# Kernel optimization log

Hardware: AMD Instinct MI355X
Metric: run time of the kernel (lower is better)

Reference implementation:

```python
import jax, jax.numpy as jnp
import numpy as np

EPS = 1e-6
CHUNK = 128  # chunk size for the causal linear-attention scan


def elu_plus_one(x):
    return jax.nn.elu(x) + 1.0


def causal_linear_attention(q, k, v):
    # out_t = (sq_t @ cumsum_{j<=t} sk_j v_j^T) / (sq_t . cumsum_{j<=t} sk_j), clamped
    B, S, D = q.shape
    sq = elu_plus_one(q)
    sk = elu_plus_one(k)
    N = S // CHUNK
    # [N, B, C, D] chunked layout for scan over chunks
    sq_c = sq.reshape(B, N, CHUNK, D).transpose(1, 0, 2, 3)
    sk_c = sk.reshape(B, N, CHUNK, D).transpose(1, 0, 2, 3)
    v_c = v.reshape(B, N, CHUNK, D).transpose(1, 0, 2, 3)
    mask = jnp.tril(jnp.ones((CHUNK, CHUNK), dtype=q.dtype))  # inclusive causal

    def step(carry, inp):
        S_kv, z = carry  # [B,D,D], [B,D] running sums from previous chunks
        sqi, ski, vi = inp
        A = jnp.einsum('bid,bjd->bij', sqi, ski) * mask  # intra-chunk causal scores
        num = jnp.einsum('bij,bje->bie', A, vi) + jnp.einsum('bid,bde->bie', sqi, S_kv)
        den = A.sum(-1) + jnp.einsum('bid,bd->bi', sqi, z)
        out = num / jnp.clip(den, EPS, None)[..., None]
        S_kv = S_kv + jnp.einsum('bcd,bce->bde', ski, vi)
        z = z + ski.sum(axis=1)
        return (S_kv, z), out

    init = (jnp.zeros((B, D, D), q.dtype), jnp.zeros((B, D), q.dtype))
    _, outs = jax.lax.scan(step, init, (sq_c, sk_c, v_c))
    return outs.transpose(1, 0, 2, 3).reshape(B, S, D)


def setup_inputs() -> dict:
    key = jax.random.key(0)
    ks = jax.random.split(key, 8)
    B, S, D = 2, 2048, 1024
    scale = 1.0 / np.sqrt(D)  # realistic init scale for the D x D projections
    return {
        'hidden_states': jax.random.normal(ks[0], (B, S, D), jnp.float32),
        'w_q': jax.random.normal(ks[1], (D, D), jnp.float32) * scale,
        'w_k': jax.random.normal(ks[2], (D, D), jnp.float32) * scale,
        'w_v': jax.random.normal(ks[3], (D, D), jnp.float32) * scale,
        'w_o': jax.random.normal(ks[4], (D, D), jnp.float32) * scale,
        'gate': jnp.zeros((1,), jnp.float32),
        'memory': jax.random.uniform(ks[5], (D, D), jnp.float32) * 0.01,
        'memory_norm': jax.random.uniform(ks[6], (D,), jnp.float32),
    }


def reference(hidden_states, w_q, w_k, w_v, w_o, gate, memory, memory_norm):
    # Projections (torch Linear: x @ W^T)
    q = hidden_states @ w_q.T
    k = hidden_states @ w_k.T
    v = hidden_states @ w_v.T

    # Retrieve from compressive memory (single bank)
    sigma_q = elu_plus_one(q)
    a_mem = sigma_q @ memory
    norm = jnp.clip(sigma_q @ memory_norm, EPS, None)[..., None]
    active = (memory_norm.sum() >= EPS).astype(q.dtype)
    memory_output = active * (a_mem / norm)

    local_output = causal_linear_attention(q, k, v)

    g = jax.nn.sigmoid(gate)  # [1], broadcasts
    output = g * memory_output + (1.0 - g) * local_output
    return output @ w_o.T
```

## Files before the change

### kernel.cpp

```cpp
#include <hip/hip_runtime.h>
#include <cstddef>

#define EPSF 1e-6f

constexpr int D   = 1024;
constexpr int Bv  = 2;
constexpr int S   = 2048;
constexpr int M   = Bv * S;
constexpr int CH  = 256;
constexpr int NCH = S / CH;

constexpr int TSZ  = 128 * 32;
constexpr int TA64 = 64 * 32;

typedef __attribute__((ext_vector_type(8))) short short8;
typedef __attribute__((ext_vector_type(4))) float floatx4;

__device__ __forceinline__ float elu1(float x) { return x > 0.f ? x + 1.f : __expf(x); }
__device__ __forceinline__ float sigmoidf_(float x) { return 1.f / (1.f + __expf(-x)); }
__device__ __forceinline__ unsigned short f2bf(float x) {
    unsigned u = __float_as_uint(x);
    return (unsigned short)((u + 0x7fffu + ((u >> 16) & 1u)) >> 16);
}
__device__ __forceinline__ float bf2f(unsigned short h) {
    return __uint_as_float(((unsigned)h) << 16);
}
__device__ __forceinline__ float wave_reduce(float x) {
#pragma unroll
    for (int off = 32; off > 0; off >>= 1) x += __shfl_down(x, off);
    return x;
}

__device__ __forceinline__ void gl_lds16(const unsigned short* g, unsigned short* l) {
    __builtin_amdgcn_global_load_lds(
        (const __attribute__((address_space(1))) void*)g,
        (__attribute__((address_space(3))) void*)l, 16, 0, 0);
}

__device__ __forceinline__ void stage128x32(const unsigned short* g, int stride,
                                            unsigned short* lds, int wave, int lane) {
    const int t   = (wave << 6) + lane;
    const int row = t >> 2;
    const int cb  = (t & 3) << 3;
    unsigned short* l0 = lds + (wave << 9);
    gl_lds16(g + (size_t)row * stride + cb, l0);
    gl_lds16(g + (size_t)(row + 64) * stride + cb, l0 + 2048);
}

__device__ __forceinline__ void stage64x32(const unsigned short* g, int stride,
                                           unsigned short* lds, int wave, int lane) {
    const int t   = (wave << 6) + lane;
    const int row = t >> 2;
    const int cb  = (t & 3) << 3;
    gl_lds16(g + (size_t)row * stride + cb, lds + (wave << 9));
}

__device__ __forceinline__ void mfma_step(const unsigned short* As, const unsigned short* Bs,
                                          int wm, int wn, int fr, int fo, floatx4 acc[4][4]) {
    short8 af[4], bf[4];
#pragma unroll
    for (int i = 0; i < 4; ++i) af[i] = *(const short8*)&As[(wm + i * 16 + fr) * 32 + fo];
#pragma unroll
    for (int j = 0; j < 4; ++j) bf[j] = *(const short8*)&Bs[(wn + j * 16 + fr) * 32 + fo];
#pragma unroll
    for (int i = 0; i < 4; ++i)
#pragma unroll
        for (int j = 0; j < 4; ++j)
            acc[i][j] = __builtin_amdgcn_mfma_f32_16x16x32_bf16(af[i], bf[j], acc[i][j], 0, 0, 0);
}

__device__ __forceinline__ void mfma_step64d(const unsigned short* As, const unsigned short* Bs,
                                             int wm, int wn, int fr, int fo,
                                             floatx4 acc[2][4], floatx4 accd[2], short8 bones) {
    short8 af[2], bf[4];
#pragma unroll
    for (int i = 0; i < 2; ++i) af[i] = *(const short8*)&As[(wm + i * 16 + fr) * 32 + fo];
#pragma unroll
    for (int j = 0; j < 4; ++j) bf[j] = *(const short8*)&Bs[(wn + j * 16 + fr) * 32 + fo];
#pragma unroll
    for (int i = 0; i < 2; ++i) {
#pragma unroll
        for (int j = 0; j < 4; ++j)
            acc[i][j] = __builtin_amdgcn_mfma_f32_16x16x32_bf16(af[i], bf[j], acc[i][j], 0, 0, 0);
        accd[i] = __builtin_amdgcn_mfma_f32_16x16x32_bf16(af[i], bones, accd[i], 0, 0, 0);
    }
}

__device__ __forceinline__ void mfma_step64(const unsigned short* As, const unsigned short* Bs,
                                            int wm, int wn, int fr, int fo, floatx4 acc[2][4]) {
    short8 af[2], bf[4];
#pragma unroll
    for (int i = 0; i < 2; ++i) af[i] = *(const short8*)&As[(wm + i * 16 + fr) * 32 + fo];
#pragma unroll
    for (int j = 0; j < 4; ++j) bf[j] = *(const short8*)&Bs[(wn + j * 16 + fr) * 32 + fo];
#pragma unroll
    for (int i = 0; i < 2; ++i)
#pragma unroll
        for (int j = 0; j < 4; ++j)
            acc[i][j] = __builtin_amdgcn_mfma_f32_16x16x32_bf16(af[i], bf[j], acc[i][j], 0, 0, 0);
}

__device__ __forceinline__ void gemm_loop_db(const unsigned short* Ag, int strideA,
                                             const unsigned short* Bg, int strideB, int Kk,
                                             unsigned short* As, unsigned short* Bs,
                                             int wave, int lane, int wm, int wn, int fr, int fo,
                                             floatx4 acc[4][4]) {
    __syncthreads();
    stage128x32(Ag, strideA, As, wave, lane);
    stage128x32(Bg, strideB, Bs, wave, lane);
    int buf = 0;
    for (int k0 = 32; k0 < Kk; k0 += 32) {
        __syncthreads();
        const int nb = buf ^ 1;
        stage128x32(Ag + k0, strideA, As + nb * TSZ, wave, lane);
        stage128x32(Bg + k0, strideB, Bs + nb * TSZ, wave, lane);
        mfma_step(As + buf * TSZ, Bs + buf * TSZ, wm, wn, fr, fo, acc);
        buf = nb;
    }
    __syncthreads();
    mfma_step(As + buf * TSZ, Bs + buf * TSZ, wm, wn, fr, fo, acc);
}

__device__ __forceinline__ void gemm_loop_db64d(const unsigned short* Ag, int strideA,
                                                const unsigned short* Bg, int strideB, int Kk,
                                                unsigned short* As, unsigned short* Bs,
                                                int wave, int lane, int wm, int wn, int fr, int fo,
                                                floatx4 acc[2][4], floatx4 accd[2], short8 bones) {
    __syncthreads();
    stage64x32(Ag, strideA, As, wave, lane);
    stage128x32(Bg, strideB, Bs, wave, lane);
    int buf = 0;
    for (int k0 = 32; k0 < Kk; k0 += 32) {
        __syncthreads();
        const int nb = buf ^ 1;
        stage64x32(Ag + k0, strideA, As + nb * TA64, wave, lane);
        stage128x32(Bg + k0, strideB, Bs + nb * TSZ, wave, lane);
        mfma_step64d(As + buf * TA64, Bs + buf * TSZ, wm, wn, fr, fo, acc, accd, bones);
        buf = nb;
    }
    __syncthreads();
    mfma_step64d(As + buf * TA64, Bs + buf * TSZ, wm, wn, fr, fo, acc, accd, bones);
}

__device__ __forceinline__ void gemm_loop_db64(const unsigned short* Ag, int strideA,
                                               const unsigned short* Bg, int strideB, int Kk,
                                               unsigned short* As, unsigned short* Bs,
                                               int wave, int lane, int wm, int wn, int fr, int fo,
                                               floatx4 acc[2][4]) {
    __syncthreads();
    stage64x32(Ag, strideA, As, wave, lane);
    stage128x32(Bg, strideB, Bs, wave, lane);
    int buf = 0;
    for (int k0 = 32; k0 < Kk; k0 += 32) {
        __syncthreads();
        const int nb = buf ^ 1;
        stage64x32(Ag + k0, strideA, As + nb * TA64, wave, lane);
        stage128x32(Bg + k0, strideB, Bs + nb * TSZ, wave, lane);
        mfma_step64(As + buf * TA64, Bs + buf * TSZ, wm, wn, fr, fo, acc);
        buf = nb;
    }
    __syncthreads();
    mfma_step64(As + buf * TA64, Bs + buf * TSZ, wm, wn, fr, fo, acc);
}

__global__ __launch_bounds__(256) void prep(const float* __restrict__ h,
                                            const float* __restrict__ w_q, const float* __restrict__ w_k,
                                            const float* __restrict__ w_v, const float* __restrict__ w_o,
                                            const float* __restrict__ memory,
                                            unsigned short* __restrict__ h_b,
                                            unsigned short* __restrict__ wq_b, unsigned short* __restrict__ wk_b,
                                            unsigned short* __restrict__ wv_b, unsigned short* __restrict__ wo_b,
                                            unsigned short* __restrict__ memT)
{
    __shared__ unsigned short T[64][72];
    const int id = blockIdx.x, tid = threadIdx.x;
    if (id < 4096) {
        const size_t i = ((size_t)id * 256 + tid) * 4;
        float4 v = *(const float4*)(h + i);
        ushort4 o; o.x = f2bf(v.x); o.y = f2bf(v.y); o.z = f2bf(v.z); o.w = f2bf(v.w);
        *(ushort4*)(h_b + i) = o;
    } else if (id < 8192) {
        const int t = id - 4096, which = t >> 10;
        const float* in = (which == 0) ? w_q : (which == 1) ? w_k : (which == 2) ? w_v : w_o;
        unsigned short* out = (which == 0) ? wq_b : (which == 1) ? wk_b : (which == 2) ? wv_b : wo_b;
        const size_t i = ((size_t)(t & 1023) * 256 + tid) * 4;
        float4 v = *(const float4*)(in + i);
        ushort4 o; o.x = f2bf(v.x); o.y = f2bf(v.y); o.z = f2bf(v.z); o.w = f2bf(v.w);
        *(ushort4*)(out + i) = o;
    } else {
        const int t = id - 8192;
        const int d0 = (t >> 4) * 64, e0 = (t & 15) * 64;
        const int r = tid >> 4, c4 = (tid & 15) * 4;
        for (int rr = r; rr < 64; rr += 16) {
            float4 v = *(const float4*)(memory + (size_t)(d0 + rr) * D + e0 + c4);
            T[rr][c4 + 0] = f2bf(v.x); T[rr][c4 + 1] = f2bf(v.y);
            T[rr][c4 + 2] = f2bf(v.z); T[rr][c4 + 3] = f2bf(v.w);
        }
        __syncthreads();
        for (int rr = r; rr < 64; rr += 16) {
            ushort4 o;
            o.x = T[c4 + 0][rr]; o.y = T[c4 + 1][rr];
            o.z = T[c4 + 2][rr]; o.w = T[c4 + 3][rr];
            *(ushort4*)(memT + (size_t)(e0 + rr) * D + d0 + c4) = o;
        }
    }
}

__global__ __launch_bounds__(256) void proj_fused(const unsigned short* __restrict__ h_b,
                                                  const unsigned short* __restrict__ wq,
                                                  const unsigned short* __restrict__ wk,
                                                  const unsigned short* __restrict__ wv,
                                                  unsigned short* __restrict__ sq,
                                                  unsigned short* __restrict__ sk,
                                                  unsigned short* __restrict__ v)
{
    __shared__ unsigned short As[2 * TSZ], Bs[2 * TSZ];
    const int id = blockIdx.x;
    const int x = id & 7, y = id >> 3;
    const int strip = x + 8 * (y % 12);
    const int n     = y / 12;
    const int sub = strip >> 5, m = strip & 31;
    const int m0 = m * 128, n0 = n * 128;
    const unsigned short* B = (sub == 0) ? wq : (sub == 1) ? wk : wv;
    unsigned short* C = (sub == 0) ? sq : (sub == 1) ? sk : v;

    const int tid = threadIdx.x, wave = tid >> 6, lane = tid & 63;
    const int wm = (wave >> 1) * 64, wn = (wave & 1) * 64;
    const int fr = lane & 15, fo = (lane >> 4) * 8;
    const int q4 = (lane >> 4) * 4;

    floatx4 acc[4][4] = {};
    gemm_loop_db(h_b + (size_t)m0 * D, D, B + (size_t)n0 * D, D, D,
                 As, Bs, wave, lane, wm, wn, fr, fo, acc);

#pragma unroll
    for (int i = 0; i < 4; ++i)
#pragma unroll
        for (int j = 0; j < 4; ++j) {
            const int col = n0 + wn + j * 16 + fr;
#pragma unroll
            for (int r = 0; r < 4; ++r) {
                const int row = m0 + wm + i * 16 + q4 + r;
                float val = acc[i][j][r];
                if (sub < 2) val = elu1(val);
                C[(size_t)row * D + col] = f2bf(val);
            }
        }
}

__global__ __launch_bounds__(256) void stage2(const unsigned short* __restrict__ sq,
                                              const unsigned short* __restrict__ sk,
                                              const unsigned short* __restrict__ memT,
                                              const unsigned short* __restrict__ v_b,
                                              const float* __restrict__ mnorm,
                                              const float* __restrict__ gate,
                                              unsigned short* __restrict__ combm,
                                              unsigned short* __restrict__ Sbuf2,
                                              unsigned short* __restrict__ vT,
                                              float* __restrict__ rowscale)
{
    __shared__ unsigned short As[2 * TSZ], Bs[2 * TSZ];
    const int id = blockIdx.x, tid = threadIdx.x;
    const int wave = tid >> 6, lane = tid & 63;
    const int wm = (wave >> 1) * 64, wn = (wave & 1) * 64;
    const int fr = lane & 15, fo = (lane >> 4) * 8;
    const int q4 = (lane >> 4) * 4;

    if (id < 256) {
        const int x = id & 7, y = id >> 3;
        const int m0 = (x + 8 * (y & 3)) * 128;
        const int n0 = (y >> 2) * 128;
        floatx4 acc[4][4] = {};
        gemm_loop_db(sq + (size_t)m0 * D, D, memT + (size_t)n0 * D, D, D,
                     As, Bs, wave, lane, wm, wn, fr, fo, acc);
#pragma unroll
        for (int i = 0; i < 4; ++i)
#pragma unroll
            for (int j = 0; j < 4; ++j) {
                const int col = n0 + wn + j * 16 + fr;
#pragma unroll
                for (int r = 0; r < 4; ++r)
                    combm[(size_t)(m0 + wm + i * 16 + q4 + r) * D + col] = f2bf(acc[i][j][r]);
            }
    } else if (id < 544) {
        const int t = id - 256;
        const int b = t / 144, rem = t % 144;
        const int p = rem >> 2, tt = rem & 3;
        const int it = tt >> 1, jt = tt & 1;
        int c = 0;
        while ((c + 1) * (c + 2) / 2 <= p) ++c;
        const int j = p - c * (c + 1) / 2;
        unsigned short* Srow0 = Sbuf2 + (size_t)(b * NCH + c) * CH * S;

        if (j == c && jt > it) {
            const int row = it * 128 + (tid >> 1);
            unsigned short* zp = Srow0 + (size_t)row * S + j * CH + jt * 128 + (tid & 1) * 64;
            uint4 z4 = make_uint4(0, 0, 0, 0);
#pragma unroll
            for (int i = 0; i < 8; ++i) *(uint4*)(zp + i * 8) = z4;
            return;
        }
        floatx4 acc[4][4] = {};
        gemm_loop_db(sq + ((size_t)b * S + (size_t)c * CH + it * 128) * D, D,
                     sk + ((size_t)b * S + (size_t)j * CH + jt * 128) * D, D, D,
                     As, Bs, wave, lane, wm, wn, fr, fo, acc);
        const bool diag = (j == c && it == jt);
#pragma unroll
        for (int i = 0; i < 4; ++i)
#pragma unroll
            for (int jj = 0; jj < 4; ++jj) {
                const int col = jt * 128 + wn + jj * 16 + fr;
#pragma unroll
                for (int r = 0; r < 4; ++r) {
                    const int row = it * 128 + wm + i * 16 + q4 + r;
                    float val = acc[i][jj][r];
                    if (diag && col > row) val = 0.f;
                    Srow0[(size_t)row * S + j * CH + col] = f2bf(val);
                }
            }
    } else if (id < 1568) {
        unsigned short (*T)[72] = (unsigned short(*)[72])As;
        const int t = id - 544;
        const int b = t >> 9, rem = t & 511;
        const int s0 = (rem >> 4) * 64, d0 = (rem & 15) * 64;
        const int r = tid >> 4, c4 = (tid & 15) * 4;
        const unsigned short* ip = v_b + (size_t)b * S * D;
        for (int rr = r; rr < 64; rr += 16) {
            ushort4 vv = *(const ushort4*)(ip + (size_t)(s0 + rr) * D + d0 + c4);
            T[rr][c4 + 0] = vv.x; T[rr][c4 + 1] = vv.y; T[rr][c4 + 2] = vv.z; T[rr][c4 + 3] = vv.w;
        }
        __syncthreads();
        unsigned short* op = vT + (size_t)b * D * S;
        for (int rr = r; rr < 64; rr += 16) {
            ushort4 o;
            o.x = T[c4 + 0][rr]; o.y = T[c4 + 1][rr];
            o.z = T[c4 + 2][rr]; o.w = T[c4 + 3][rr];
            *(ushort4*)(op + (size_t)(d0 + rr) * S + s0 + c4) = o;
        }
    } else {
        const int row = (id - 1568) * 4 + wave;
        const unsigned short* sr = sq + (size_t)row * D;
        float dot = 0.f, msum = 0.f;
        for (int d = lane; d < D; d += 64) {
            float mn = mnorm[d];
            dot += bf2f(sr[d]) * mn;
            msum += mn;
        }
        dot = wave_reduce(dot);
        msum = wave_reduce(msum);
        if (lane == 0) {
            const float g = sigmoidf_(gate[0]);
            const float active = (msum >= EPSF) ? 1.f : 0.f;
            rowscale[row] = g * active / fmaxf(dot, EPSF);
        }
    }
}

__global__ __launch_bounds__(256) void pv64(const unsigned short* __restrict__ Sbuf2,
                                            const unsigned short* __restrict__ vT,
                                            const float* __restrict__ rowscale,
                                            const float* __restrict__ gate,
                                            unsigned short* __restrict__ combm)
{
    __shared__ unsigned short As2[2 * TA64], Bs2[2 * TSZ];
    const int id = blockIdx.x, tid = threadIdx.x;
    const int wave = tid >> 6, lane = tid & 63;
    const int wm = (wave >> 1) * 32, wn = (wave & 1) * 64;
    const int fr = lane & 15, fo = (lane >> 4) * 8;
    const int q4 = (lane >> 4) * 4;

    const int x = id & 7, y = id >> 3;
    const int g_ = x + 8 * (y & 7);
    const int e  = y >> 3;
    const int b = g_ >> 5;
    const int rem = g_ & 31;
    const int c = (NCH - 1) - (rem >> 2);
    const int i0 = (rem & 3) * 64, e0 = e * 128;

    const short one_bf = (short)0x3F80;
    short8 bones = {one_bf, one_bf, one_bf, one_bf, one_bf, one_bf, one_bf, one_bf};

    floatx4 acc[2][4] = {};
    floatx4 accd[2] = {};
    gemm_loop_db64d(Sbuf2 + ((size_t)(b * NCH + c) * CH + i0) * S, S,
                    vT + (size_t)b * D * S + (size_t)e0 * S, S, (c + 1) * CH,
                    As2, Bs2, wave, lane, wm, wn, fr, fo, acc, accd, bones);

    const float g = sigmoidf_(gate[0]);
    const float wloc = 1.f - g;
#pragma unroll
    for (int i = 0; i < 2; ++i)
#pragma unroll
        for (int j = 0; j < 4; ++j) {
            const int col = e0 + wn + j * 16 + fr;
#pragma unroll
            for (int r = 0; r < 4; ++r) {
                const int li = i0 + wm + i * 16 + q4 + r;
                const int rg = b * S + c * CH + li;
                const float inv = wloc / fmaxf(accd[i][r], EPSF);
                const size_t idx = (size_t)rg * D + col;
                combm[idx] = f2bf(bf2f(combm[idx]) * rowscale[rg] + acc[i][j][r] * inv);
            }
        }
}

__global__ __launch_bounds__(256) void outproj64(const unsigned short* __restrict__ A,
                                                 const unsigned short* __restrict__ wo,
                                                 float* __restrict__ out)
{
    __shared__ unsigned short As2[2 * TA64], Bs2[2 * TSZ];
    const int id = blockIdx.x, tid = threadIdx.x;
    const int wave = tid >> 6, lane = tid & 63;
    const int wm = (wave >> 1) * 32, wn = (wave & 1) * 64;
    const int fr = lane & 15, fo = (lane >> 4) * 8;
    const int q4 = (lane >> 4) * 4;

    const int x = id & 7, y = id >> 3;
    const int m0 = (x + 8 * (y & 7)) * 64;
    const int n0 = (y >> 3) * 128;

    floatx4 acc[2][4] = {};
    gemm_loop_db64(A + (size_t)m0 * D, D, wo + (size_t)n0 * D, D, D,
                   As2, Bs2, wave, lane, wm, wn, fr, fo, acc);

#pragma unroll
    for (int i = 0; i < 2; ++i)
#pragma unroll
        for (int j = 0; j < 4; ++j) {
            const int col = n0 + wn + j * 16 + fr;
#pragma unroll
            for (int r = 0; r < 4; ++r)
                out[(size_t)(m0 + wm + i * 16 + q4 + r) * D + col] = acc[i][j][r];
        }
}

extern "C" void kernel_launch(void* const* d_in, const int* in_sizes, int n_in,
                              void* d_out, int out_size, void* d_ws, size_t ws_size,
                              hipStream_t stream)
{
    const float* h      = (const float*)d_in[0];
    const float* w_q    = (const float*)d_in[1];
    const float* w_k    = (const float*)d_in[2];
    const float* w_v    = (const float*)d_in[3];
    const float* w_o    = (const float*)d_in[4];
    const float* gate   = (const float*)d_in[5];
    const float* memory = (const float*)d_in[6];
    const float* mnorm  = (const float*)d_in[7];
    float* out = (float*)d_out;

    unsigned short* h_b   = (unsigned short*)d_ws;
    unsigned short* wq_b  = h_b + (size_t)M * D;
    unsigned short* wk_b  = wq_b + (size_t)D * D;
    unsigned short* wv_b  = wk_b + (size_t)D * D;
    unsigned short* wo_b  = wv_b + (size_t)D * D;
    unsigned short* memT  = wo_b + (size_t)D * D;
    unsigned short* sq_b  = memT + (size_t)D * D;
    unsigned short* sk_b  = sq_b + (size_t)M * D;
    unsigned short* v_b   = sk_b + (size_t)M * D;
    unsigned short* vT    = v_b + (size_t)M * D;
    unsigned short* Sbuf2 = vT + (size_t)M * D;
    unsigned short* combm = Sbuf2 + (size_t)Bv * NCH * CH * S;
    float* rowscale = (float*)(combm + (size_t)M * D);

    dim3 blk(256);

    prep<<<8448, blk, 0, stream>>>(h, w_q, w_k, w_v, w_o, memory,
                                   h_b, wq_b, wk_b, wv_b, wo_b, memT);
    proj_fused<<<768, blk, 0, stream>>>(h_b, wq_b, wk_b, wv_b, sq_b, sk_b, v_b);
    stage2<<<2592, blk, 0, stream>>>(sq_b, sk_b, memT, v_b, mnorm, gate,
                                     combm, Sbuf2, vT, rowscale);
    pv64<<<512, blk, 0, stream>>>(Sbuf2, vT, rowscale, gate, combm);
    outproj64<<<512, blk, 0, stream>>>(combm, wo_b, out);
}
```

Baseline: 230.1 us.

## Double K-tile depth to 64 with XOR-swizzled LDS layout in all GEMMs

Every GEMM main loop now advances K by 64 per stage instead of 32, which halves the number of barriers and loop iterations. The staging writes each 16-byte chunk into a column position XOR-swizzled by row so that fragment reads with a 64-element row stride avoid LDS bank conflicts. The cost is double the LDS footprint per block, which may lower occupancy, plus a longer prologue and epilogue per tile.

```diff
diff --git a/kernel.cpp b/kernel.cpp
--- a/kernel.cpp
+++ b/kernel.cpp
@@ -10,8 +10,8 @@
 constexpr int CH  = 256;
 constexpr int NCH = S / CH;
 
-constexpr int TSZ  = 128 * 32;
-constexpr int TA64 = 64 * 32;
+constexpr int TSZ  = 128 * 64;
+constexpr int TA64 = 64 * 64;
 
 typedef __attribute__((ext_vector_type(8))) short short8;
 typedef __attribute__((ext_vector_type(4))) float floatx4;
@@ -37,130 +37,152 @@
         (__attribute__((address_space(3))) void*)l, 16, 0, 0);
 }
 
-__device__ __forceinline__ void stage128x32(const unsigned short* g, int stride,
+
+__device__ __forceinline__ void stage128x64(const unsigned short* g, int stride,
                                             unsigned short* lds, int wave, int lane) {
-    const int t   = (wave << 6) + lane;
-    const int row = t >> 2;
-    const int cb  = (t & 3) << 3;
-    unsigned short* l0 = lds + (wave << 9);
-    gl_lds16(g + (size_t)row * stride + cb, l0);
-    gl_lds16(g + (size_t)(row + 64) * stride + cb, l0 + 2048);
-}
-
-__device__ __forceinline__ void stage64x32(const unsigned short* g, int stride,
+    const int base = (wave << 6) + lane;
+    const int c8   = (lane & 7) ^ (lane >> 3);
+#pragma unroll
+    for (int q = 0; q < 4; ++q) {
+        const int P   = (q << 8) + base;
+        const int row = P >> 3;
+        gl_lds16(g + (size_t)row * stride + (c8 << 3), lds + (q << 11) + (wave << 9));
+    }
+}
+
+__device__ __forceinline__ void stage64x64(const unsigned short* g, int stride,
                                            unsigned short* lds, int wave, int lane) {
-    const int t   = (wave << 6) + lane;
-    const int row = t >> 2;
-    const int cb  = (t & 3) << 3;
-    gl_lds16(g + (size_t)row * stride + cb, lds + (wave << 9));
+    const int base = (wave << 6) + lane;
+    const int c8   = (lane & 7) ^ (lane >> 3);
+#pragma unroll
+    for (int q = 0; q < 2; ++q) {
+        const int P   = (q << 8) + base;
+        const int row = P >> 3;
+        gl_lds16(g + (size_t)row * stride + (c8 << 3), lds + (q << 11) + (wave << 9));
+    }
 }
 
 __device__ __forceinline__ void mfma_step(const unsigned short* As, const unsigned short* Bs,
-                                          int wm, int wn, int fr, int fo, floatx4 acc[4][4]) {
-    short8 af[4], bf[4];
-#pragma unroll
-    for (int i = 0; i < 4; ++i) af[i] = *(const short8*)&As[(wm + i * 16 + fr) * 32 + fo];
-#pragma unroll
-    for (int j = 0; j < 4; ++j) bf[j] = *(const short8*)&Bs[(wn + j * 16 + fr) * 32 + fo];
-#pragma unroll
-    for (int i = 0; i < 4; ++i)
-#pragma unroll
-        for (int j = 0; j < 4; ++j)
-            acc[i][j] = __builtin_amdgcn_mfma_f32_16x16x32_bf16(af[i], bf[j], acc[i][j], 0, 0, 0);
+                                          int wm, int wn, int fr, int g, floatx4 acc[4][4]) {
+    const int x7 = fr & 7;
+#pragma unroll
+    for (int s = 0; s < 2; ++s) {
+        const int off = ((g + 4 * s) ^ x7) << 3;
+        short8 af[4], bf[4];
+#pragma unroll
+        for (int i = 0; i < 4; ++i) af[i] = *(const short8*)&As[(wm + i * 16 + fr) * 64 + off];
+#pragma unroll
+        for (int j = 0; j < 4; ++j) bf[j] = *(const short8*)&Bs[(wn + j * 16 + fr) * 64 + off];
+#pragma unroll
+        for (int i = 0; i < 4; ++i)
+#pragma unroll
+            for (int j = 0; j < 4; ++j)
+                acc[i][j] = __builtin_amdgcn_mfma_f32_16x16x32_bf16(af[i], bf[j], acc[i][j], 0, 0, 0);
+    }
 }
 
 __device__ __forceinline__ void mfma_step64d(const unsigned short* As, const unsigned short* Bs,
-                                             int wm, int wn, int fr, int fo,
+                                             int wm, int wn, int fr, int g,
                                              floatx4 acc[2][4], floatx4 accd[2], short8 bones) {
-    short8 af[2], bf[4];
-#pragma unroll
-    for (int i = 0; i < 2; ++i) af[i] = *(const short8*)&As[(wm + i * 16 + fr) * 32 + fo];
-#pragma unroll
-    for (int j = 0; j < 4; ++j) bf[j] = *(const short8*)&Bs[(wn + j * 16 + fr) * 32 + fo];
-#pragma unroll
-    for (int i = 0; i < 2; ++i) {
-#pragma unroll
-        for (int j = 0; j < 4; ++j)
-            acc[i][j] = __builtin_amdgcn_mfma_f32_16x16x32_bf16(af[i], bf[j], acc[i][j], 0, 0, 0);
-        accd[i] = __builtin_amdgcn_mfma_f32_16x16x32_bf16(af[i], bones, accd[i], 0, 0, 0);
+    const int x7 = fr & 7;
+#pragma unroll
+    for (int s = 0; s < 2; ++s) {
+        const int off = ((g + 4 * s) ^ x7) << 3;
+        short8 af[2], bf[4];
+#pragma unroll
+        for (int i = 0; i < 2; ++i) af[i] = *(const short8*)&As[(wm + i * 16 + fr) * 64 + off];
+#pragma unroll
+        for (int j = 0; j < 4; ++j) bf[j] = *(const short8*)&Bs[(wn + j * 16 + fr) * 64 + off];
+#pragma unroll
+        for (int i = 0; i < 2; ++i) {
+#pragma unroll
+            for (int j = 0; j < 4; ++j)
+                acc[i][j] = __builtin_amdgcn_mfma_f32_16x16x32_bf16(af[i], bf[j], acc[i][j], 0, 0, 0);
+            accd[i] = __builtin_amdgcn_mfma_f32_16x16x32_bf16(af[i], bones, accd[i], 0, 0, 0);
+        }
     }
 }
 
 __device__ __forceinline__ void mfma_step64(const unsigned short* As, const unsigned short* Bs,
-                                            int wm, int wn, int fr, int fo, floatx4 acc[2][4]) {
-    short8 af[2], bf[4];
-#pragma unroll
-    for (int i = 0; i < 2; ++i) af[i] = *(const short8*)&As[(wm + i * 16 + fr) * 32 + fo];
-#pragma unroll
-    for (int j = 0; j < 4; ++j) bf[j] = *(const short8*)&Bs[(wn + j * 16 + fr) * 32 + fo];
-#pragma unroll
-    for (int i = 0; i < 2; ++i)
-#pragma unroll
-        for (int j = 0; j < 4; ++j)
-            acc[i][j] = __builtin_amdgcn_mfma_f32_16x16x32_bf16(af[i], bf[j], acc[i][j], 0, 0, 0);
+                                            int wm, int wn, int fr, int g, floatx4 acc[2][4]) {
+    const int x7 = fr & 7;
+#pragma unroll
+    for (int s = 0; s < 2; ++s) {
+        const int off = ((g + 4 * s) ^ x7) << 3;
+        short8 af[2], bf[4];
+#pragma unroll
+        for (int i = 0; i < 2; ++i) af[i] = *(const short8*)&As[(wm + i * 16 + fr) * 64 + off];
+#pragma unroll
+        for (int j = 0; j < 4; ++j) bf[j] = *(const short8*)&Bs[(wn + j * 16 + fr) * 64 + off];
+#pragma unroll
+        for (int i = 0; i < 2; ++i)
+#pragma unroll
+            for (int j = 0; j < 4; ++j)
+                acc[i][j] = __builtin_amdgcn_mfma_f32_16x16x32_bf16(af[i], bf[j], acc[i][j], 0, 0, 0);
+    }
 }
 
 __device__ __forceinline__ void gemm_loop_db(const unsigned short* Ag, int strideA,
                                              const unsigned short* Bg, int strideB, int Kk,
                                              unsigned short* As, unsigned short* Bs,
-                                             int wave, int lane, int wm, int wn, int fr, int fo,
+                                             int wave, int lane, int wm, int wn, int fr, int g,
                                              floatx4 acc[4][4]) {
     __syncthreads();
-    stage128x32(Ag, strideA, As, wave, lane);
-    stage128x32(Bg, strideB, Bs, wave, lane);
+    stage128x64(Ag, strideA, As, wave, lane);
+    stage128x64(Bg, strideB, Bs, wave, lane);
     int buf = 0;
-    for (int k0 = 32; k0 < Kk; k0 += 32) {
+    for (int k0 = 64; k0 < Kk; k0 += 64) {
         __syncthreads();
         const int nb = buf ^ 1;
-        stage128x32(Ag + k0, strideA, As + nb * TSZ, wave, lane);
-        stage128x32(Bg + k0, strideB, Bs + nb * TSZ, wave, lane);
-        mfma_step(As + buf * TSZ, Bs + buf * TSZ, wm, wn, fr, fo, acc);
+        stage128x64(Ag + k0, strideA, As + nb * TSZ, wave, lane);
+        stage128x64(Bg + k0, strideB, Bs + nb * TSZ, wave, lane);
+        mfma_step(As + buf * TSZ, Bs + buf * TSZ, wm, wn, fr, g, acc);
         buf = nb;
     }
     __syncthreads();
-    mfma_step(As + buf * TSZ, Bs + buf * TSZ, wm, wn, fr, fo, acc);
+    mfma_step(As + buf * TSZ, Bs + buf * TSZ, wm, wn, fr, g, acc);
 }
 
 __device__ __forceinline__ void gemm_loop_db64d(const unsigned short* Ag, int strideA,
                                                 const unsigned short* Bg, int strideB, int Kk,
                                                 unsigned short* As, unsigned short* Bs,
-                                                int wave, int lane, int wm, int wn, int fr, int fo,
+                                                int wave, int lane, int wm, int wn, int fr, int g,
                                                 floatx4 acc[2][4], floatx4 accd[2], short8 bones) {
     __syncthreads();
-    stage64x32(Ag, strideA, As, wave, lane);
-    stage128x32(Bg, strideB, Bs, wave, lane);
+    stage64x64(Ag, strideA, As, wave, lane);
+    stage128x64(Bg, strideB, Bs, wave, lane);
     int buf = 0;
-    for (int k0 = 32; k0 < Kk; k0 += 32) {
+    for (int k0 = 64; k0 < Kk; k0 += 64) {
         __syncthreads();
         const int nb = buf ^ 1;
-        stage64x32(Ag + k0, strideA, As + nb * TA64, wave, lane);
-        stage128x32(Bg + k0, strideB, Bs + nb * TSZ, wave, lane);
-        mfma_step64d(As + buf * TA64, Bs + buf * TSZ, wm, wn, fr, fo, acc, accd, bones);
+        stage64x64(Ag + k0, strideA, As + nb * TA64, wave, lane);
+        stage128x64(Bg + k0, strideB, Bs + nb * TSZ, wave, lane);
+        mfma_step64d(As + buf * TA64, Bs + buf * TSZ, wm, wn, fr, g, acc, accd, bones);
         buf = nb;
     }
     __syncthreads();
-    mfma_step64d(As + buf * TA64, Bs + buf * TSZ, wm, wn, fr, fo, acc, accd, bones);
+    mfma_step64d(As + buf * TA64, Bs + buf * TSZ, wm, wn, fr, g, acc, accd, bones);
 }
 
 __device__ __forceinline__ void gemm_loop_db64(const unsigned short* Ag, int strideA,
                                                const unsigned short* Bg, int strideB, int Kk,
                                                unsigned short* As, unsigned short* Bs,
-                                               int wave, int lane, int wm, int wn, int fr, int fo,
+                                               int wave, int lane, int wm, int wn, int fr, int g,
                                                floatx4 acc[2][4]) {
     __syncthreads();
-    stage64x32(Ag, strideA, As, wave, lane);
-    stage128x32(Bg, strideB, Bs, wave, lane);
+    stage64x64(Ag, strideA, As, wave, lane);
+    stage128x64(Bg, strideB, Bs, wave, lane);
     int buf = 0;
-    for (int k0 = 32; k0 < Kk; k0 += 32) {
+    for (int k0 = 64; k0 < Kk; k0 += 64) {
         __syncthreads();
         const int nb = buf ^ 1;
-        stage64x32(Ag + k0, strideA, As + nb * TA64, wave, lane);
-        stage128x32(Bg + k0, strideB, Bs + nb * TSZ, wave, lane);
-        mfma_step64(As + buf * TA64, Bs + buf * TSZ, wm, wn, fr, fo, acc);
+        stage64x64(Ag + k0, strideA, As + nb * TA64, wave, lane);
+        stage128x64(Bg + k0, strideB, Bs + nb * TSZ, wave, lane);
+        mfma_step64(As + buf * TA64, Bs + buf * TSZ, wm, wn, fr, g, acc);
         buf = nb;
     }
     __syncthreads();
-    mfma_step64(As + buf * TA64, Bs + buf * TSZ, wm, wn, fr, fo, acc);
+    mfma_step64(As + buf * TA64, Bs + buf * TSZ, wm, wn, fr, g, acc);
 }
 
 __global__ __launch_bounds__(256) void prep(const float* __restrict__ h,
@@ -226,12 +248,12 @@
 
     const int tid = threadIdx.x, wave = tid >> 6, lane = tid & 63;
     const int wm = (wave >> 1) * 64, wn = (wave & 1) * 64;
-    const int fr = lane & 15, fo = (lane >> 4) * 8;
-    const int q4 = (lane >> 4) * 4;
+    const int fr = lane & 15, g = lane >> 4;
+    const int q4 = g * 4;
 
     floatx4 acc[4][4] = {};
     gemm_loop_db(h_b + (size_t)m0 * D, D, B + (size_t)n0 * D, D, D,
-                 As, Bs, wave, lane, wm, wn, fr, fo, acc);
+                 As, Bs, wave, lane, wm, wn, fr, g, acc);
 
 #pragma unroll
     for (int i = 0; i < 4; ++i)
@@ -263,8 +285,8 @@
     const int id = blockIdx.x, tid = threadIdx.x;
     const int wave = tid >> 6, lane = tid & 63;
     const int wm = (wave >> 1) * 64, wn = (wave & 1) * 64;
-    const int fr = lane & 15, fo = (lane >> 4) * 8;
-    const int q4 = (lane >> 4) * 4;
+    const int fr = lane & 15, g = lane >> 4;
+    const int q4 = g * 4;
 
     if (id < 256) {
         const int x = id & 7, y = id >> 3;
@@ -272,7 +294,7 @@
         const int n0 = (y >> 2) * 128;
         floatx4 acc[4][4] = {};
         gemm_loop_db(sq + (size_t)m0 * D, D, memT + (size_t)n0 * D, D, D,
-                     As, Bs, wave, lane, wm, wn, fr, fo, acc);
+                     As, Bs, wave, lane, wm, wn, fr, g, acc);
 #pragma unroll
         for (int i = 0; i < 4; ++i)
 #pragma unroll
@@ -303,7 +325,7 @@
         floatx4 acc[4][4] = {};
         gemm_loop_db(sq + ((size_t)b * S + (size_t)c * CH + it * 128) * D, D,
                      sk + ((size_t)b * S + (size_t)j * CH + jt * 128) * D, D, D,
-                     As, Bs, wave, lane, wm, wn, fr, fo, acc);
+                     As, Bs, wave, lane, wm, wn, fr, g, acc);
         const bool diag = (j == c && it == jt);
 #pragma unroll
         for (int i = 0; i < 4; ++i)
@@ -349,9 +371,9 @@
         dot = wave_reduce(dot);
         msum = wave_reduce(msum);
         if (lane == 0) {
-            const float g = sigmoidf_(gate[0]);
+            const float gg = sigmoidf_(gate[0]);
             const float active = (msum >= EPSF) ? 1.f : 0.f;
-            rowscale[row] = g * active / fmaxf(dot, EPSF);
+            rowscale[row] = gg * active / fmaxf(dot, EPSF);
         }
     }
 }
@@ -366,8 +388,8 @@
     const int id = blockIdx.x, tid = threadIdx.x;
     const int wave = tid >> 6, lane = tid & 63;
     const int wm = (wave >> 1) * 32, wn = (wave & 1) * 64;
-    const int fr = lane & 15, fo = (lane >> 4) * 8;
-    const int q4 = (lane >> 4) * 4;
+    const int fr = lane & 15, g = lane >> 4;
+    const int q4 = g * 4;
 
     const int x = id & 7, y = id >> 3;
     const int g_ = x + 8 * (y & 7);
@@ -384,10 +406,10 @@
     floatx4 accd[2] = {};
     gemm_loop_db64d(Sbuf2 + ((size_t)(b * NCH + c) * CH + i0) * S, S,
                     vT + (size_t)b * D * S + (size_t)e0 * S, S, (c + 1) * CH,
-                    As2, Bs2, wave, lane, wm, wn, fr, fo, acc, accd, bones);
-
-    const float g = sigmoidf_(gate[0]);
-    const float wloc = 1.f - g;
+                    As2, Bs2, wave, lane, wm, wn, fr, g, acc, accd, bones);
+
+    const float gg = sigmoidf_(gate[0]);
+    const float wloc = 1.f - gg;
 #pragma unroll
     for (int i = 0; i < 2; ++i)
 #pragma unroll
@@ -412,8 +434,8 @@
     const int id = blockIdx.x, tid = threadIdx.x;
     const int wave = tid >> 6, lane = tid & 63;
     const int wm = (wave >> 1) * 32, wn = (wave & 1) * 64;
-    const int fr = lane & 15, fo = (lane >> 4) * 8;
-    const int q4 = (lane >> 4) * 4;
+    const int fr = lane & 15, g = lane >> 4;
+    const int q4 = g * 4;
 
     const int x = id & 7, y = id >> 3;
     const int m0 = (x + 8 * (y & 7)) * 64;
@@ -421,7 +443,7 @@
 
     floatx4 acc[2][4] = {};
     gemm_loop_db64(A + (size_t)m0 * D, D, wo + (size_t)n0 * D, D, D,
-                   As2, Bs2, wave, lane, wm, wn, fr, fo, acc);
+                   As2, Bs2, wave, lane, wm, wn, fr, g, acc);
 
 #pragma unroll
     for (int i = 0; i < 2; ++i)
```

Result: slower. 244.5 us (+6.3%).
